# Kernel tuning notes

Hardware: AMD Instinct MI355X
Metric: run time of the kernel (lower is better)

Reference implementation:

```python
import jax, jax.numpy as jnp
import numpy as np

B, L, D, N_HEADS = 8, 512, 1024, 16
D_HEAD = D // N_HEADS


def _mha_fuzzy(x_q, x_k, x_v, Wq, bq, Wk, bk, Wv, bv, Wo, bo):
    """Multi-head fuzzy attention, product t-norm score function."""
    b, lq, d_model = x_q.shape
    lk = x_k.shape[1]

    def proj(x, W, bias, l):
        # [b, l, D] -> [b, h, l, d_head]
        return (x @ W + bias).reshape(b, l, N_HEADS, D_HEAD).transpose(0, 2, 1, 3)

    Q = proj(x_q, Wq, bq, lq)
    K = proj(x_k, Wk, bk, lk)
    V = proj(x_v, Wv, bv, lk)
    # fuzzy memberships in [0,1]
    mu_q = jax.nn.sigmoid(Q)
    mu_k = jax.nn.sigmoid(K)
    # product t-norm aggregated over feature dim (mean), then softmax normalize
    scores = jnp.einsum('bhid,bhjd->bhij', mu_q, mu_k) / D_HEAD  # [b,h,lq,lk]
    attn = jax.nn.softmax(scores, axis=-1)
    out = jnp.einsum('bhij,bhjd->bhid', attn, V)
    out = out.transpose(0, 2, 1, 3).reshape(b, lq, d_model)
    return out @ Wo + bo, attn.mean(axis=1)  # avg over heads


def setup_inputs() -> dict:
    key = jax.random.key(0)
    ks = jax.random.split(key, 16)
    s = 1.0 / np.sqrt(D)
    inp = {
        'text_features': jax.random.normal(ks[0], (B, L, D), jnp.float32),
        'image_features': jax.random.normal(ks[1], (B, L, D), jnp.float32),
        'Wq': jax.random.normal(ks[2], (D, D), jnp.float32) * s,
        'bq': jnp.zeros((D,), jnp.float32),
        'Wk': jax.random.normal(ks[3], (D, D), jnp.float32) * s,
        'bk': jnp.zeros((D,), jnp.float32),
        'Wv': jax.random.normal(ks[4], (D, D), jnp.float32) * s,
        'bv': jnp.zeros((D,), jnp.float32),
        'Wo': jax.random.normal(ks[5], (D, D), jnp.float32) * s,
        'bo': jnp.zeros((D,), jnp.float32),
        'W1': jax.random.normal(ks[6], (3 * D, D), jnp.float32) * (1.0 / np.sqrt(3 * D)),
        'b1': jnp.zeros((D,), jnp.float32),
        'W2': jax.random.normal(ks[7], (D, D), jnp.float32) * s,
        'b2': jnp.zeros((D,), jnp.float32),
    }
    return inp


def reference(text_features, image_features, Wq, bq, Wk, bk, Wv, bv, Wo, bo, W1, b1, W2, b2):
    # shared fuzzy attention module applied in both cross-modal directions
    text_cross, avg_attn = _mha_fuzzy(text_features, image_features, image_features,
                                      Wq, bq, Wk, bk, Wv, bv, Wo, bo)
    image_cross, _ = _mha_fuzzy(image_features, text_features, text_features,
                                Wq, bq, Wk, bk, Wv, bv, Wo, bo)
    combined = jnp.concatenate([text_features, image_features, text_cross], axis=-1)
    hidden = jax.nn.relu(combined @ W1 + b1)
    compositional_output = hidden @ W2 + b2
    return text_cross, image_cross, compositional_output, avg_attn
```

## Files before the change

### kernel.cpp

```cpp
#include <hip/hip_runtime.h>

#define NB 8
#define SL 512
#define DM 1024
#define NH 16
#define DH 64

using bfrag = __attribute__((ext_vector_type(8))) short;
using facc  = __attribute__((ext_vector_type(4))) float;

__device__ __forceinline__ float bf2f(ushort u) {
    return __uint_as_float(((unsigned)u) << 16);
}
__device__ __forceinline__ ushort f2bf(float f) {
    unsigned x = __float_as_uint(f);
    return (ushort)((x + 0x7FFFu + ((x >> 16) & 1u)) >> 16);
}
__device__ __forceinline__ float4 bf4_f4(ushort4 u) {
    return make_float4(bf2f(u.x), bf2f(u.y), bf2f(u.z), bf2f(u.w));
}
__device__ __forceinline__ unsigned pack2(float a, float b) {
    return (unsigned)f2bf(a) | ((unsigned)f2bf(b) << 16);
}
__device__ __forceinline__ void gload16(const ushort* g, ushort* l) {
    __builtin_amdgcn_global_load_lds(
        (const __attribute__((address_space(1))) unsigned*)g,
        (__attribute__((address_space(3))) unsigned*)l, 16, 0, 0);
}

__global__ __launch_bounds__(256)
void cvt_k(const float* __restrict__ s, ushort* __restrict__ d) {
    const size_t i = (size_t)(blockIdx.x * 256 + threadIdx.x) * 4;
    const float4 f = *(const float4*)(s + i);
    *(ushort4*)(d + i) = make_ushort4(f2bf(f.x), f2bf(f.y), f2bf(f.z), f2bf(f.w));
}

__global__ __launch_bounds__(256)
void tconv_k(const float* __restrict__ W, ushort* __restrict__ WT,
             const int R, const int C) {
    __shared__ ushort T[64][68];
    const int tid = threadIdx.x;
    const int c0 = blockIdx.x * 64, r0 = blockIdx.y * 64;
    #pragma unroll
    for (int rr = 0; rr < 4; ++rr) {
        const int r = (tid >> 4) + rr * 16;
        const int c4 = (tid & 15) * 4;
        const float4 f = *(const float4*)(W + (size_t)(r0 + r) * C + c0 + c4);
        T[c4+0][r] = f2bf(f.x); T[c4+1][r] = f2bf(f.y);
        T[c4+2][r] = f2bf(f.z); T[c4+3][r] = f2bf(f.w);
    }
    __syncthreads();
    #pragma unroll
    for (int rr = 0; rr < 4; ++rr) {
        const int c = (tid >> 4) + rr * 16;
        const int r4 = (tid & 15) * 4;
        *(ushort4*)(WT + (size_t)(c0 + c) * R + r0 + r4) =
            make_ushort4(T[c][r4+0], T[c][r4+1], T[c][r4+2], T[c][r4+3]);
    }
}

template<int ACT, int OMODE>
__global__ __launch_bounds__(256, 2)
void mfma_gemm(const ushort* __restrict__ A0, const ushort* __restrict__ A1,
               const float* __restrict__ A2f,
               const int KA1, const int KA2, const int Ktot,
               const int lda, const int ldaf,
               const ushort* __restrict__ AM1, const int Msplit,
               const ushort* __restrict__ BT, const int ldb,
               const float* __restrict__ bias, const float* __restrict__ biasK,
               const float* __restrict__ biasV,
               float* __restrict__ outf, ushort* __restrict__ outb,
               ushort* __restrict__ outbK, ushort* __restrict__ outbVT,
               const int clustN)
{
    __shared__ ushort sh[32768];
    const int tid  = threadIdx.x;
    const int w    = tid >> 6;
    const int lane = tid & 63;
    const int ln   = lane & 15, qd = lane >> 4;
    const int wm = (w & 1) * 64, wn = (w >> 1) * 64;

    const int NTg = gridDim.x, MTg = gridDim.y;
    const int L   = blockIdx.x + NTg * blockIdx.y;
    const int xcd = L & 7, sIdx = L >> 3;
    int mt, nt;
    if (clustN) { const int np = NTg >> 3; nt = xcd * np + sIdx % np; mt = sIdx / np; }
    else        { mt = xcd * (MTg >> 3) + sIdx / NTg; nt = sIdx - (sIdx / NTg) * NTg; }
    const int m0 = mt * 128, n0 = nt * 128;

    const ushort* A0u = A0; const ushort* A1u = A1; int m0A = m0;
    if (Msplit && m0 >= Msplit) { A0u = AM1; A1u = AM1; m0A = m0 - Msplit; }

    const int arow = (lane >> 3);
    const int kc8s = ((lane & 7) ^ arow) * 8;

    facc acc[4][4];
    #pragma unroll
    for (int i = 0; i < 4; ++i)
        #pragma unroll
        for (int j = 0; j < 4; ++j)
            acc[i][j] = (facc){0.f, 0.f, 0.f, 0.f};

    auto stage = [&](int k0, ushort* buf) {
        ushort* Asb = buf;
        ushort* Bsb = buf + 8192;
        #pragma unroll
        for (int t = 0; t < 4; ++t) {
            const int c = w * 4 + t;
            gload16(BT + (size_t)(n0 + c * 8 + arow) * ldb + k0 + kc8s,
                    &Bsb[c * 512]);
        }
        if (k0 < KA2) {
            const ushort* Ab; int ko;
            if (k0 < KA1) { Ab = A0u; ko = k0; }
            else          { Ab = A1u; ko = k0 - KA1; }
            #pragma unroll
            for (int t = 0; t < 4; ++t) {
                const int c = w * 4 + t;
                gload16(Ab + (size_t)(m0A + c * 8 + arow) * lda + ko + kc8s,
                        &Asb[c * 512]);
            }
        } else {
            const int ko = k0 - KA2;
            #pragma unroll
            for (int t = 0; t < 4; ++t) {
                const int c = w * 4 + t;
                const float* src = A2f + (size_t)(m0A + c * 8 + arow) * ldaf + ko + kc8s;
                const float4 f0 = *(const float4*)src;
                const float4 f1 = *(const float4*)(src + 4);
                uint4 p;
                p.x = pack2(f0.x, f0.y); p.y = pack2(f0.z, f0.w);
                p.z = pack2(f1.x, f1.y); p.w = pack2(f1.z, f1.w);
                *(uint4*)&Asb[c * 512 + lane * 8] = p;
            }
        }
    };

    stage(0, sh);
    for (int k0 = 0; k0 < Ktot; k0 += 64) {
        ushort* cur = sh + ((k0 >> 6) & 1) * 16384;
        ushort* nxt = sh + (((k0 >> 6) & 1) ^ 1) * 16384;
        __syncthreads();
        if (k0 + 64 < Ktot) stage(k0 + 64, nxt);
        ushort* Asb = cur;
        ushort* Bsb = cur + 8192;
        #pragma unroll
        for (int ks = 0; ks < 2; ++ks) {
            const int ch = (ks * 4 + qd) ^ (ln & 7);
            bfrag af[4], bfv[4];
            #pragma unroll
            for (int i = 0; i < 4; ++i)
                af[i] = *(const bfrag*)&Asb[(wm + i*16 + ln) * 64 + ch * 8];
            #pragma unroll
            for (int j = 0; j < 4; ++j)
                bfv[j] = *(const bfrag*)&Bsb[(wn + j*16 + ln) * 64 + ch * 8];
            #pragma unroll
            for (int i = 0; i < 4; ++i)
                #pragma unroll
                for (int j = 0; j < 4; ++j)
                    acc[i][j] = __builtin_amdgcn_mfma_f32_16x16x32_bf16(
                        af[i], bfv[j], acc[i][j], 0, 0, 0);
        }
    }

    if (OMODE == 4) {
        const int seg   = n0 >> 10;
        const int nloc0 = n0 & 1023;
        const float* bs = (seg == 0) ? bias : (seg == 1) ? biasK : biasV;
        if (seg < 2) {
            ushort* ob = (seg == 0) ? outb : outbK;
            #pragma unroll
            for (int j = 0; j < 4; ++j) {
                const int nl = nloc0 + wn + j * 16 + ln;
                const float bn = bs[nl];
                #pragma unroll
                for (int i = 0; i < 4; ++i) {
                    const int mb = m0 + wm + i * 16 + qd * 4;
                    #pragma unroll
                    for (int r = 0; r < 4; ++r) {
                        const float v = 1.f / (1.f + __expf(-(acc[i][j][r] + bn)));
                        const int m = mb + r;
                        const int g = m >> 9, l = m & 511;
                        ob[(((size_t)(g * NH + (nl >> 6))) * SL + l) * DH + (nl & 63)]
                            = f2bf(v);
                    }
                }
            }
        } else {
            __syncthreads();
            #pragma unroll
            for (int j = 0; j < 4; ++j) {
                const int n_l = wn + j * 16 + ln;
                const float bn = bs[nloc0 + n_l];
                #pragma unroll
                for (int i = 0; i < 4; ++i) {
                    #pragma unroll
                    for (int r = 0; r < 4; ++r) {
                        const int m_l = wm + i * 16 + qd * 4 + r;
                        const int c = (m_l >> 3) ^ (n_l & 7);
                        sh[n_l * 128 + c * 8 + (m_l & 7)] = f2bf(acc[i][j][r] + bn);
                    }
                }
            }
            __syncthreads();
            const int n_l = tid >> 1, half = tid & 1;
            const int nl = nloc0 + n_l;
            const int g = m0 >> 9, l0 = m0 & 511;
            ushort* dst = outbVT +
                (((size_t)(g * NH + (nl >> 6))) * DH + (nl & 63)) * SL + l0;
            #pragma unroll
            for (int u = 0; u < 8; ++u) {
                const int c = half * 8 + u;
                const int cs = c ^ (n_l & 7);
                *(uint4*)(dst + c * 8) = *(const uint4*)&sh[n_l * 128 + cs * 8];
            }
        }
        return;
    }

    #pragma unroll
    for (int j = 0; j < 4; ++j) {
        const int n = n0 + wn + j * 16 + ln;
        const float bn = bias[n];
        #pragma unroll
        for (int i = 0; i < 4; ++i) {
            const int mb = m0 + wm + i * 16 + qd * 4;
            #pragma unroll
            for (int r = 0; r < 4; ++r) {
                float v = acc[i][j][r] + bn;
                if (ACT == 1)      v = 1.f / (1.f + __expf(-v));
                else if (ACT == 2) v = v > 0.f ? v : 0.f;
                const int m = mb + r;
                if (OMODE == 0) outf[(size_t)m * DM + n] = v;
                else            outb[(size_t)m * DM + n] = f2bf(v);
            }
        }
    }
}

__global__ __launch_bounds__(256, 2)
void attn2_k(const ushort* __restrict__ Qm, const ushort* __restrict__ Km,
             const ushort* __restrict__ VTm, ushort* __restrict__ AO,
             float* __restrict__ RS)
{
    __shared__ ushort Ks[128 * 64];
    __shared__ ushort VTs[64 * 128];
    __shared__ ushort Es[128 * 128];
    const int tid  = threadIdx.x;
    const int w    = tid >> 6;
    const int lane = tid & 63;
    const int ln   = lane & 15, qd = lane >> 4;
    const int wm  = (w & 1) * 64;
    const int wns = (w >> 1) * 64;
    const int wnd = (w >> 1) * 32;
    const int qt = blockIdx.x, h = blockIdx.y, b = blockIdx.z;
    const size_t ho = ((size_t)(b * NH + h)) * SL * DH;
    const ushort* Qg  = Qm  + ho + (size_t)qt * 128 * DH;
    const ushort* Kg  = Km  + ho;
    const ushort* VTg = VTm + ho;

    bfrag qf[4][2];
    #pragma unroll
    for (int i = 0; i < 4; ++i)
        #pragma unroll
        for (int ks = 0; ks < 2; ++ks)
            qf[i][ks] = *(const bfrag*)(Qg + (size_t)(wm + i*16 + ln) * DH + ks*32 + qd*8);

    facc oacc[4][2];
    #pragma unroll
    for (int i = 0; i < 4; ++i)
        #pragma unroll
        for (int j = 0; j < 2; ++j)
            oacc[i][j] = (facc){0.f, 0.f, 0.f, 0.f};
    float rp[4][4];
    #pragma unroll
    for (int i = 0; i < 4; ++i)
        #pragma unroll
        for (int r = 0; r < 4; ++r)
            rp[i][r] = 0.f;

    const int arow = lane >> 3;
    const int kc8s = ((lane & 7) ^ arow) * 8;
    const int vrow = lane >> 4;

    for (int kc = 0; kc < 4; ++kc) {
        __syncthreads();
        #pragma unroll
        for (int t = 0; t < 4; ++t) {
            const int c = w * 4 + t;
            const int vc8s = ((lane & 15) ^ ((c * 4 + vrow) & 7)) * 8;
            gload16(Kg + (size_t)(kc*128 + c*8 + arow) * DH + kc8s, &Ks[c * 512]);
            gload16(VTg + (size_t)(c*4 + vrow) * SL + kc*128 + vc8s, &VTs[c * 512]);
        }
        __syncthreads();

        facc sacc[4][4];
        #pragma unroll
        for (int i = 0; i < 4; ++i)
            #pragma unroll
            for (int j = 0; j < 4; ++j)
                sacc[i][j] = (facc){0.f, 0.f, 0.f, 0.f};
        #pragma unroll
        for (int ks = 0; ks < 2; ++ks) {
            const int ch = (ks * 4 + qd) ^ (ln & 7);
            bfrag kf[4];
            #pragma unroll
            for (int j = 0; j < 4; ++j)
                kf[j] = *(const bfrag*)&Ks[(wns + j*16 + ln) * 64 + ch * 8];
            #pragma unroll
            for (int i = 0; i < 4; ++i)
                #pragma unroll
                for (int j = 0; j < 4; ++j)
                    sacc[i][j] = __builtin_amdgcn_mfma_f32_16x16x32_bf16(
                        qf[i][ks], kf[j], sacc[i][j], 0, 0, 0);
        }

        #pragma unroll
        for (int i = 0; i < 4; ++i) {
            #pragma unroll
            for (int r = 0; r < 4; ++r) {
                const int q = wm + i*16 + qd*4 + r;
                float p = 0.f;
                #pragma unroll
                for (int j = 0; j < 4; ++j) {
                    const float e = __expf(sacc[i][j][r] * 0.015625f);
                    const int key = wns + j*16 + ln;
                    const int c = (key >> 3) ^ (q & 7);
                    Es[q * 128 + c * 8 + (key & 7)] = f2bf(e);
                    p += e;
                }
                p += __shfl_xor(p, 1, 16);
                p += __shfl_xor(p, 2, 16);
                p += __shfl_xor(p, 4, 16);
                p += __shfl_xor(p, 8, 16);
                rp[i][r] += p;
            }
        }
        __syncthreads();

        #pragma unroll
        for (int ks2 = 0; ks2 < 4; ++ks2) {
            const int vch = (ks2 * 4 + qd) ^ (ln & 7);
            bfrag ea[4], vb[2];
            #pragma unroll
            for (int i = 0; i < 4; ++i) {
                const int q = wm + i*16 + ln;
                const int cs = (ks2*4 + qd) ^ (q & 7);
                ea[i] = *(const bfrag*)&Es[q * 128 + cs * 8];
            }
            #pragma unroll
            for (int j = 0; j < 2; ++j)
                vb[j] = *(const bfrag*)&VTs[(wnd + j*16 + ln) * 128 + vch * 8];
            #pragma unroll
            for (int i = 0; i < 4; ++i)
                #pragma unroll
                for (int j = 0; j < 2; ++j)
                    oacc[i][j] = __builtin_amdgcn_mfma_f32_16x16x32_bf16(
                        ea[i], vb[j], oacc[i][j], 0, 0, 0);
        }
    }

    __syncthreads();
    float* rsls = (float*)Ks;
    if (ln == 0) {
        #pragma unroll
        for (int i = 0; i < 4; ++i)
            #pragma unroll
            for (int r = 0; r < 4; ++r)
                rsls[(w >> 1) * 128 + wm + i*16 + qd*4 + r] = rp[i][r];
    }
    __syncthreads();
    if (tid < 128) {
        const float t = rsls[tid] + rsls[128 + tid];
        RS[(size_t)(b * NH + h) * SL + qt * 128 + tid] = t;
        rsls[tid] = t;
    }
    __syncthreads();

    #pragma unroll
    for (int i = 0; i < 4; ++i) {
        #pragma unroll
        for (int r = 0; r < 4; ++r) {
            const int q = wm + i*16 + qd*4 + r;
            const float inv = 1.f / rsls[q];
            const size_t rowo = ((size_t)(b*SL + qt*128 + q)) * DM + h*DH;
            #pragma unroll
            for (int j = 0; j < 2; ++j)
                AO[rowo + wnd + j*16 + ln] = f2bf(oacc[i][j][r] * inv);
        }
    }
}

__global__ __launch_bounds__(256, 2)
void avg3_k(const ushort* __restrict__ Qm, const ushort* __restrict__ Km,
            const float* __restrict__ RS, float* __restrict__ avga)
{
    __shared__ ushort Qs[64 * 64];
    __shared__ ushort Kt[64 * 64];
    __shared__ float rss[64];
    const int tid  = threadIdx.x;
    const int w    = tid >> 6;
    const int lane = tid & 63;
    const int ln   = lane & 15, qd = lane >> 4;
    const int wq = (w & 1) * 32, wk = (w >> 1) * 32;
    const int kt = blockIdx.x, qt = blockIdx.y, b = blockIdx.z;

    const int arow = lane >> 3;
    const int kc8s = ((lane & 7) ^ arow) * 8;

    float acc[2][2][4];
    #pragma unroll
    for (int i = 0; i < 2; ++i)
        #pragma unroll
        for (int j = 0; j < 2; ++j)
            #pragma unroll
            for (int r = 0; r < 4; ++r)
                acc[i][j][r] = 0.f;

    for (int h = 0; h < NH; ++h) {
        const size_t ho = ((size_t)(b * NH + h)) * SL * DH;
        __syncthreads();
        #pragma unroll
        for (int t = 0; t < 2; ++t) {
            const int c = w * 2 + t;
            gload16(Qm + ho + (size_t)(qt*64 + c*8 + arow) * DH + kc8s, &Qs[c * 512]);
            gload16(Km + ho + (size_t)(kt*64 + c*8 + arow) * DH + kc8s, &Kt[c * 512]);
        }
        if (tid < 64) rss[tid] = RS[(size_t)(b*NH + h)*SL + qt*64 + tid];
        __syncthreads();

        facc s[2][2];
        #pragma unroll
        for (int i = 0; i < 2; ++i)
            #pragma unroll
            for (int j = 0; j < 2; ++j)
                s[i][j] = (facc){0.f, 0.f, 0.f, 0.f};
        #pragma unroll
        for (int ks = 0; ks < 2; ++ks) {
            const int ch = (ks * 4 + qd) ^ (ln & 7);
            bfrag qa[2], kb[2];
            #pragma unroll
            for (int i = 0; i < 2; ++i)
                qa[i] = *(const bfrag*)&Qs[(wq + i*16 + ln) * 64 + ch * 8];
            #pragma unroll
            for (int j = 0; j < 2; ++j)
                kb[j] = *(const bfrag*)&Kt[(wk + j*16 + ln) * 64 + ch * 8];
            #pragma unroll
            for (int i = 0; i < 2; ++i)
                #pragma unroll
                for (int j = 0; j < 2; ++j)
                    s[i][j] = __builtin_amdgcn_mfma_f32_16x16x32_bf16(
                        qa[i], kb[j], s[i][j], 0, 0, 0);
        }
        #pragma unroll
        for (int i = 0; i < 2; ++i) {
            #pragma unroll
            for (int r = 0; r < 4; ++r) {
                const float ir = 0.0625f / rss[wq + i*16 + qd*4 + r];
                #pragma unroll
                for (int j = 0; j < 2; ++j)
                    acc[i][j][r] += __expf(s[i][j][r] * 0.015625f) * ir;
            }
        }
    }
    #pragma unroll
    for (int i = 0; i < 2; ++i) {
        #pragma unroll
        for (int r = 0; r < 4; ++r) {
            const int q = wq + i*16 + qd*4 + r;
            #pragma unroll
            for (int j = 0; j < 2; ++j)
                avga[((size_t)(b*SL + qt*64 + q)) * SL + kt*64 + wk + j*16 + ln]
                    = acc[i][j][r];
        }
    }
}

extern "C" void kernel_launch(void* const* d_in, const int* in_sizes, int n_in,
                              void* d_out, int out_size, void* d_ws, size_t ws_size,
                              hipStream_t stream)
{
    (void)in_sizes; (void)n_in; (void)out_size; (void)ws_size;
    const float* text  = (const float*)d_in[0];
    const float* image = (const float*)d_in[1];
    const float* Wq = (const float*)d_in[2];
    const float* bq = (const float*)d_in[3];
    const float* Wk = (const float*)d_in[4];
    const float* bk = (const float*)d_in[5];
    const float* Wv = (const float*)d_in[6];
    const float* bv = (const float*)d_in[7];
    const float* Wo = (const float*)d_in[8];
    const float* bo = (const float*)d_in[9];
    const float* W1 = (const float*)d_in[10];
    const float* b1 = (const float*)d_in[11];
    const float* W2 = (const float*)d_in[12];
    const float* b2 = (const float*)d_in[13];
    float* out = (float*)d_out;

    const size_t SZ   = (size_t)NB * SL * DM;
    const size_t HALF = SZ;

    ushort* xbf = (ushort*)d_ws;
    ushort* Qb  = xbf + 2*SZ;
    ushort* Kb  = Qb  + 2*SZ;
    ushort* VT  = Kb  + 2*SZ;
    ushort* AOt = VT  + 2*SZ;
    ushort* Wt  = AOt + SZ;
    float*  RS  = (float*)(Wt + 3*DM*DM);
    ushort* AOi    = VT + HALF;
    ushort* hidden = Qb;

    float* text_cross = out;
    float* comp       = out + 2*SZ;
    float* avga       = out + 3*SZ;

    const dim3 blk(256);

    cvt_k<<<4096, blk, 0, stream>>>(text,  xbf);
    cvt_k<<<4096, blk, 0, stream>>>(image, xbf + SZ);

    tconv_k<<<dim3(16,16), blk, 0, stream>>>(Wq, Wt,           DM, DM);
    tconv_k<<<dim3(16,16), blk, 0, stream>>>(Wk, Wt + DM*DM,   DM, DM);
    tconv_k<<<dim3(16,16), blk, 0, stream>>>(Wv, Wt + 2*DM*DM, DM, DM);
    mfma_gemm<0,4><<<dim3(24,64), blk, 0, stream>>>(
        xbf, xbf, nullptr, DM, DM, DM, DM, DM, nullptr, 0,
        Wt, DM, bq, bk, bv, nullptr, Qb, Kb, VT, 1);

    attn2_k<<<dim3(SL/128, NH, NB), blk, 0, stream>>>(Qb, Kb + HALF, VT + HALF, AOt, RS);
    avg3_k<<<dim3(SL/64, SL/64, NB), blk, 0, stream>>>(Qb, Kb + HALF, RS, avga);
    attn2_k<<<dim3(SL/128, NH, NB), blk, 0, stream>>>(Qb + HALF, Kb, VT, AOi, RS);

    tconv_k<<<dim3(16,16), blk, 0, stream>>>(Wo, Wt, DM, DM);
    mfma_gemm<0,0><<<dim3(8,64), blk, 0, stream>>>(
        AOt, AOt, nullptr, DM, DM, DM, DM, DM, AOi, 4096,
        Wt, DM, bo, nullptr, nullptr, text_cross, nullptr, nullptr, nullptr, 0);

    tconv_k<<<dim3(16,48), blk, 0, stream>>>(W1, Wt, 3*DM, DM);
    mfma_gemm<2,2><<<dim3(8,32), blk, 0, stream>>>(
        xbf, xbf + SZ, text_cross, DM, 2*DM, 3*DM, DM, DM, nullptr, 0,
        Wt, 3*DM, b1, nullptr, nullptr, nullptr, hidden, nullptr, nullptr, 0);
    tconv_k<<<dim3(16,16), blk, 0, stream>>>(W2, Wt, DM, DM);
    mfma_gemm<0,0><<<dim3(8,32), blk, 0, stream>>>(
        hidden, hidden, nullptr, DM, DM, DM, DM, DM, nullptr, 0,
        Wt, DM, b2, nullptr, nullptr, comp, nullptr, nullptr, nullptr, 0);
}
```

Measured before the change: 400.5 us.

## Use 64-row GEMM tiles for small GEMMs, coalesce Q/K epilogue, double-buffer avg kernel

Templates the MFMA GEMM on the M tile size and launches the two 4096-row MLP GEMMs with 64-row tiles, doubling block count so more CUs are filled. The QKV sigmoid epilogue now stages results through shared memory and writes full 128-byte rows instead of scattered 2-byte stores. The head-averaged attention kernel double-buffers its per-head Q/K tiles so the next head's loads overlap the current head's compute. The smaller tiles lower per-block reuse and the epilogue adds extra barriers.

```diff
diff --git a/kernel.cpp b/kernel.cpp
--- a/kernel.cpp
+++ b/kernel.cpp
@@ -59,8 +59,8 @@
     }
 }
 
-template<int ACT, int OMODE>
-__global__ __launch_bounds__(256, 2)
+template<int ACT, int OMODE, int BM>
+__global__ __launch_bounds__(256, (BM == 128) ? 2 : 3)
 void mfma_gemm(const ushort* __restrict__ A0, const ushort* __restrict__ A1,
                const float* __restrict__ A2f,
                const int KA1, const int KA2, const int Ktot,
@@ -73,12 +73,16 @@
                ushort* __restrict__ outbK, ushort* __restrict__ outbVT,
                const int clustN)
 {
-    __shared__ ushort sh[32768];
+    constexpr int NJ  = (BM == 128) ? 4 : 2;
+    constexpr int TA  = BM / 32;
+    constexpr int BUF = BM * 64 + 8192;
+    __shared__ ushort sh[2 * BUF];
     const int tid  = threadIdx.x;
     const int w    = tid >> 6;
     const int lane = tid & 63;
     const int ln   = lane & 15, qd = lane >> 4;
-    const int wm = (w & 1) * 64, wn = (w >> 1) * 64;
+    const int wm = (BM == 128) ? (w & 1) * 64 : 0;
+    const int wn = (BM == 128) ? (w >> 1) * 64 : w * 32;
 
     const int NTg = gridDim.x, MTg = gridDim.y;
     const int L   = blockIdx.x + NTg * blockIdx.y;
@@ -86,7 +90,7 @@
     int mt, nt;
     if (clustN) { const int np = NTg >> 3; nt = xcd * np + sIdx % np; mt = sIdx / np; }
     else        { mt = xcd * (MTg >> 3) + sIdx / NTg; nt = sIdx - (sIdx / NTg) * NTg; }
-    const int m0 = mt * 128, n0 = nt * 128;
+    const int m0 = mt * BM, n0 = nt * 128;
 
     const ushort* A0u = A0; const ushort* A1u = A1; int m0A = m0;
     if (Msplit && m0 >= Msplit) { A0u = AM1; A1u = AM1; m0A = m0 - Msplit; }
@@ -94,16 +98,16 @@
     const int arow = (lane >> 3);
     const int kc8s = ((lane & 7) ^ arow) * 8;
 
-    facc acc[4][4];
+    facc acc[4][NJ];
     #pragma unroll
     for (int i = 0; i < 4; ++i)
         #pragma unroll
-        for (int j = 0; j < 4; ++j)
+        for (int j = 0; j < NJ; ++j)
             acc[i][j] = (facc){0.f, 0.f, 0.f, 0.f};
 
     auto stage = [&](int k0, ushort* buf) {
         ushort* Asb = buf;
-        ushort* Bsb = buf + 8192;
+        ushort* Bsb = buf + BM * 64;
         #pragma unroll
         for (int t = 0; t < 4; ++t) {
             const int c = w * 4 + t;
@@ -115,16 +119,16 @@
             if (k0 < KA1) { Ab = A0u; ko = k0; }
             else          { Ab = A1u; ko = k0 - KA1; }
             #pragma unroll
-            for (int t = 0; t < 4; ++t) {
-                const int c = w * 4 + t;
+            for (int t = 0; t < TA; ++t) {
+                const int c = w * TA + t;
                 gload16(Ab + (size_t)(m0A + c * 8 + arow) * lda + ko + kc8s,
                         &Asb[c * 512]);
             }
         } else {
             const int ko = k0 - KA2;
             #pragma unroll
-            for (int t = 0; t < 4; ++t) {
-                const int c = w * 4 + t;
+            for (int t = 0; t < TA; ++t) {
+                const int c = w * TA + t;
                 const float* src = A2f + (size_t)(m0A + c * 8 + arow) * ldaf + ko + kc8s;
                 const float4 f0 = *(const float4*)src;
                 const float4 f1 = *(const float4*)(src + 4);
@@ -138,26 +142,26 @@
 
     stage(0, sh);
     for (int k0 = 0; k0 < Ktot; k0 += 64) {
-        ushort* cur = sh + ((k0 >> 6) & 1) * 16384;
-        ushort* nxt = sh + (((k0 >> 6) & 1) ^ 1) * 16384;
+        ushort* cur = sh + ((k0 >> 6) & 1) * BUF;
+        ushort* nxt = sh + (((k0 >> 6) & 1) ^ 1) * BUF;
         __syncthreads();
         if (k0 + 64 < Ktot) stage(k0 + 64, nxt);
         ushort* Asb = cur;
-        ushort* Bsb = cur + 8192;
+        ushort* Bsb = cur + BM * 64;
         #pragma unroll
         for (int ks = 0; ks < 2; ++ks) {
             const int ch = (ks * 4 + qd) ^ (ln & 7);
-            bfrag af[4], bfv[4];
+            bfrag af[4], bfv[NJ];
             #pragma unroll
             for (int i = 0; i < 4; ++i)
                 af[i] = *(const bfrag*)&Asb[(wm + i*16 + ln) * 64 + ch * 8];
             #pragma unroll
-            for (int j = 0; j < 4; ++j)
+            for (int j = 0; j < NJ; ++j)
                 bfv[j] = *(const bfrag*)&Bsb[(wn + j*16 + ln) * 64 + ch * 8];
             #pragma unroll
             for (int i = 0; i < 4; ++i)
                 #pragma unroll
-                for (int j = 0; j < 4; ++j)
+                for (int j = 0; j < NJ; ++j)
                     acc[i][j] = __builtin_amdgcn_mfma_f32_16x16x32_bf16(
                         af[i], bfv[j], acc[i][j], 0, 0, 0);
         }
@@ -169,27 +173,34 @@
         const float* bs = (seg == 0) ? bias : (seg == 1) ? biasK : biasV;
         if (seg < 2) {
             ushort* ob = (seg == 0) ? outb : outbK;
-            #pragma unroll
-            for (int j = 0; j < 4; ++j) {
-                const int nl = nloc0 + wn + j * 16 + ln;
-                const float bn = bs[nl];
+            __syncthreads();
+            #pragma unroll
+            for (int j = 0; j < NJ; ++j) {
+                const int n_l = wn + j * 16 + ln;
+                const float bn = bs[nloc0 + n_l];
                 #pragma unroll
                 for (int i = 0; i < 4; ++i) {
-                    const int mb = m0 + wm + i * 16 + qd * 4;
                     #pragma unroll
                     for (int r = 0; r < 4; ++r) {
+                        const int m_l = wm + i * 16 + qd * 4 + r;
                         const float v = 1.f / (1.f + __expf(-(acc[i][j][r] + bn)));
-                        const int m = mb + r;
-                        const int g = m >> 9, l = m & 511;
-                        ob[(((size_t)(g * NH + (nl >> 6))) * SL + l) * DH + (nl & 63)]
-                            = f2bf(v);
+                        sh[m_l * 136 + n_l] = f2bf(v);
                     }
                 }
             }
+            __syncthreads();
+            const int m_l = tid >> 1, hh = tid & 1;
+            const int m = m0 + m_l, g = m >> 9, l = m & 511;
+            ushort* dst = ob +
+                (((size_t)(g * NH + (nloc0 >> 6) + hh)) * SL + l) * DH;
+            const ushort* srow = &sh[m_l * 136 + hh * 64];
+            #pragma unroll
+            for (int c = 0; c < 8; ++c)
+                *(uint4*)(dst + c * 8) = *(const uint4*)(srow + c * 8);
         } else {
             __syncthreads();
             #pragma unroll
-            for (int j = 0; j < 4; ++j) {
+            for (int j = 0; j < NJ; ++j) {
                 const int n_l = wn + j * 16 + ln;
                 const float bn = bs[nloc0 + n_l];
                 #pragma unroll
@@ -219,7 +230,7 @@
     }
 
     #pragma unroll
-    for (int j = 0; j < 4; ++j) {
+    for (int j = 0; j < NJ; ++j) {
         const int n = n0 + wn + j * 16 + ln;
         const float bn = bias[n];
         #pragma unroll
@@ -395,9 +406,9 @@
 void avg3_k(const ushort* __restrict__ Qm, const ushort* __restrict__ Km,
             const float* __restrict__ RS, float* __restrict__ avga)
 {
-    __shared__ ushort Qs[64 * 64];
-    __shared__ ushort Kt[64 * 64];
-    __shared__ float rss[64];
+    __shared__ ushort Qs[2][64 * 64];
+    __shared__ ushort Kt[2][64 * 64];
+    __shared__ float rss[2][64];
     const int tid  = threadIdx.x;
     const int w    = tid >> 6;
     const int lane = tid & 63;
@@ -417,17 +428,24 @@
             for (int r = 0; r < 4; ++r)
                 acc[i][j][r] = 0.f;
 
-    for (int h = 0; h < NH; ++h) {
+    auto stageh = [&](int h, int pb) {
         const size_t ho = ((size_t)(b * NH + h)) * SL * DH;
-        __syncthreads();
         #pragma unroll
         for (int t = 0; t < 2; ++t) {
             const int c = w * 2 + t;
-            gload16(Qm + ho + (size_t)(qt*64 + c*8 + arow) * DH + kc8s, &Qs[c * 512]);
-            gload16(Km + ho + (size_t)(kt*64 + c*8 + arow) * DH + kc8s, &Kt[c * 512]);
-        }
-        if (tid < 64) rss[tid] = RS[(size_t)(b*NH + h)*SL + qt*64 + tid];
+            gload16(Qm + ho + (size_t)(qt*64 + c*8 + arow) * DH + kc8s,
+                    &Qs[pb][c * 512]);
+            gload16(Km + ho + (size_t)(kt*64 + c*8 + arow) * DH + kc8s,
+                    &Kt[pb][c * 512]);
+        }
+        if (tid < 64) rss[pb][tid] = RS[(size_t)(b*NH + h)*SL + qt*64 + tid];
+    };
+
+    stageh(0, 0);
+    for (int h = 0; h < NH; ++h) {
+        const int pb = h & 1;
         __syncthreads();
+        if (h + 1 < NH) stageh(h + 1, pb ^ 1);
 
         facc s[2][2];
         #pragma unroll
@@ -441,10 +459,10 @@
             bfrag qa[2], kb[2];
             #pragma unroll
             for (int i = 0; i < 2; ++i)
-                qa[i] = *(const bfrag*)&Qs[(wq + i*16 + ln) * 64 + ch * 8];
+                qa[i] = *(const bfrag*)&Qs[pb][(wq + i*16 + ln) * 64 + ch * 8];
             #pragma unroll
             for (int j = 0; j < 2; ++j)
-                kb[j] = *(const bfrag*)&Kt[(wk + j*16 + ln) * 64 + ch * 8];
+                kb[j] = *(const bfrag*)&Kt[pb][(wk + j*16 + ln) * 64 + ch * 8];
             #pragma unroll
             for (int i = 0; i < 2; ++i)
                 #pragma unroll
@@ -456,7 +474,7 @@
         for (int i = 0; i < 2; ++i) {
             #pragma unroll
             for (int r = 0; r < 4; ++r) {
-                const float ir = 0.0625f / rss[wq + i*16 + qd*4 + r];
+                const float ir = 0.0625f / rss[pb][wq + i*16 + qd*4 + r];
                 #pragma unroll
                 for (int j = 0; j < 2; ++j)
                     acc[i][j][r] += __expf(s[i][j][r] * 0.015625f) * ir;
@@ -522,7 +540,7 @@
     tconv_k<<<dim3(16,16), blk, 0, stream>>>(Wq, Wt,           DM, DM);
     tconv_k<<<dim3(16,16), blk, 0, stream>>>(Wk, Wt + DM*DM,   DM, DM);
     tconv_k<<<dim3(16,16), blk, 0, stream>>>(Wv, Wt + 2*DM*DM, DM, DM);
-    mfma_gemm<0,4><<<dim3(24,64), blk, 0, stream>>>(
+    mfma_gemm<0,4,128><<<dim3(24,64), blk, 0, stream>>>(
         xbf, xbf, nullptr, DM, DM, DM, DM, DM, nullptr, 0,
         Wt, DM, bq, bk, bv, nullptr, Qb, Kb, VT, 1);
 
@@ -531,16 +549,16 @@
     attn2_k<<<dim3(SL/128, NH, NB), blk, 0, stream>>>(Qb + HALF, Kb, VT, AOi, RS);
 
     tconv_k<<<dim3(16,16), blk, 0, stream>>>(Wo, Wt, DM, DM);
-    mfma_gemm<0,0><<<dim3(8,64), blk, 0, stream>>>(
+    mfma_gemm<0,0,128><<<dim3(8,64), blk, 0, stream>>>(
         AOt, AOt, nullptr, DM, DM, DM, DM, DM, AOi, 4096,
         Wt, DM, bo, nullptr, nullptr, text_cross, nullptr, nullptr, nullptr, 0);
 
     tconv_k<<<dim3(16,48), blk, 0, stream>>>(W1, Wt, 3*DM, DM);
-    mfma_gemm<2,2><<<dim3(8,32), blk, 0, stream>>>(
+    mfma_gemm<2,2,64><<<dim3(8,64), blk, 0, stream>>>(
         xbf, xbf + SZ, text_cross, DM, 2*DM, 3*DM, DM, DM, nullptr, 0,
         Wt, 3*DM, b1, nullptr, nullptr, nullptr, hidden, nullptr, nullptr, 0);
     tconv_k<<<dim3(16,16), blk, 0, stream>>>(W2, Wt, DM, DM);
-    mfma_gemm<0,0><<<dim3(8,32), blk, 0, stream>>>(
+    mfma_gemm<0,0,64><<<dim3(8,64), blk, 0, stream>>>(
         hidden, hidden, nullptr, DM, DM, DM, DM, DM, nullptr, 0,
         Wt, DM, b2, nullptr, nullptr, comp, nullptr, nullptr, nullptr, 0);
 }
```

After: 413.9 us. +3.4%, slower.
